# Optimization experiments

Hardware: AMD Instinct MI355X
Metric: run time of the kernel (lower is better)

Reference implementation:

```python
import jax, jax.numpy as jnp
import numpy as np

N = 100000   # n_nodes
E = 800000   # n_edges
IN = 128
HID = 128
OUT = 40
EPS = 1e-5   # BatchNorm1d eps


def setup_inputs() -> dict:
    key = jax.random.key(0)
    ks = jax.random.split(key, 16)
    def w(k, i, o):
        return jax.random.normal(k, (i, o), jnp.float32) / np.sqrt(i).astype(np.float32)
    return {
        "x": jax.random.normal(ks[0], (N, IN), jnp.float32),
        "edge_index": jax.random.randint(ks[1], (2, E), 0, N, dtype=jnp.int64),
        # SAGEConv weights: Wl acts on aggregated neighbors, Wr on root features
        "Wl0": w(ks[2], IN, HID),  "Wr0": w(ks[3], IN, HID),
        "Wl1": w(ks[4], HID, HID), "Wr1": w(ks[5], HID, HID),
        "Wl2": w(ks[6], HID, OUT), "Wr2": w(ks[7], HID, OUT),
        "b2": jnp.zeros((OUT,), jnp.float32),  # bias only on last layer
        # BatchNorm params for layers 0,1 (last layer has no BN)
        "g0": jnp.ones((HID,), jnp.float32), "be0": jnp.zeros((HID,), jnp.float32),
        "g1": jnp.ones((HID,), jnp.float32), "be1": jnp.zeros((HID,), jnp.float32),
    }


def _sage_conv(x, src, dst, Wl, Wr, b=None):
    # mean aggregation of source messages at destination nodes
    msg = x[src]                                             # [E, d] gather
    agg = jax.ops.segment_sum(msg, dst, num_segments=N)      # [N, d]
    cnt = jax.ops.segment_sum(jnp.ones((src.shape[0],), x.dtype), dst,
                              num_segments=N)                # [N]
    mean = agg / jnp.maximum(cnt, 1.0)[:, None]
    out = mean @ Wl + x @ Wr
    if b is not None:
        out = out + b
    return out


def _batch_norm(h, gamma, beta):
    # training-mode BN over node dim, biased variance (matches torch BatchNorm1d)
    mu = h.mean(axis=0)
    var = h.var(axis=0)
    return (h - mu) * jax.lax.rsqrt(var + EPS) * gamma + beta


def reference(x, edge_index, Wl0, Wr0, Wl1, Wr1, Wl2, Wr2, b2, g0, be0, g1, be1):
    src, dst = edge_index[0], edge_index[1]
    h = _sage_conv(x, src, dst, Wl0, Wr0)
    h = jax.nn.relu(_batch_norm(h, g0, be0))
    h = _sage_conv(h, src, dst, Wl1, Wr1)
    h = jax.nn.relu(_batch_norm(h, g1, be1))
    h = _sage_conv(h, src, dst, Wl2, Wr2, b2)
    return h
```

## Files before the change

### kernel.cpp

```cpp
#include <hip/hip_runtime.h>
#include <hip/hip_bf16.h>

#define N_NODES 100000
#define N_EDGES 800000
#define EPS 1e-5f
#define NBANK 32
#define HB_BLOCKS 256
#define HB_PER 3125
#define BUCKET_N 12500
#define MROW 68
#define BST 1024
#define CPT 13

typedef __attribute__((ext_vector_type(8))) short short8;
typedef __attribute__((ext_vector_type(4))) float floatx4;

__device__ __forceinline__ unsigned short f2b(float f) {
    unsigned int u = __float_as_uint(f);
    u = (u + 0x7fffu + ((u >> 16) & 1u)) >> 16;
    return (unsigned short)u;
}
__device__ __forceinline__ float blo(unsigned int u) { return __uint_as_float(u << 16); }
__device__ __forceinline__ float bhi(unsigned int u) { return __uint_as_float(u & 0xffff0000u); }
__device__ __forceinline__ float b2f(unsigned short s) {
    return __uint_as_float(((unsigned int)s) << 16);
}

__device__ __forceinline__ void pack_one(const float* __restrict__ Wl,
                                         const float* __restrict__ Wr,
                                         unsigned short* __restrict__ out,
                                         int Hreal, int NCT, int tid) {
    int i = tid & 7;
    int lane = (tid >> 3) & 63;
    int q = tid >> 9;
    int c = q % NCT;
    int t = q / NCT;
    int k = t * 32 + (lane >> 4) * 8 + i;
    int n = c * 16 + (lane & 15);
    float v = 0.f;
    if (n < Hreal) v = (k < 128) ? Wl[k * Hreal + n] : Wr[(k - 128) * Hreal + n];
    out[tid] = f2b(v);
}

__global__ void __launch_bounds__(256) prep_k(const float* __restrict__ x,
                                              unsigned short* __restrict__ o,
                                              const int* __restrict__ dst,
                                              unsigned int* __restrict__ bhist,
                                              const float* __restrict__ Wl0, const float* __restrict__ Wr0,
                                              const float* __restrict__ Wl1, const float* __restrict__ Wr1,
                                              const float* __restrict__ Wl2, const float* __restrict__ Wr2,
                                              unsigned short* __restrict__ W0p,
                                              unsigned short* __restrict__ W1p,
                                              unsigned short* __restrict__ W2p) {
    int b = blockIdx.x;
    if (b < 12500) {
        int i = b * 256 + threadIdx.x;
        float4 v = ((const float4*)x)[i];
        ushort4 r;
        r.x = f2b(v.x); r.y = f2b(v.y); r.z = f2b(v.z); r.w = f2b(v.w);
        ((ushort4*)o)[i] = r;
        return;
    }
    if (b < 12756) {
        __shared__ unsigned int lh[8];
        int hb = b - 12500;
        if (threadIdx.x < 8) lh[threadIdx.x] = 0;
        __syncthreads();
        int start = hb * HB_PER;
        for (int i = threadIdx.x; i < HB_PER; i += 256) {
            int d = dst[start + i];
            atomicAdd(&lh[(unsigned int)d / BUCKET_N], 1u);
        }
        __syncthreads();
        if (threadIdx.x < 8) bhist[threadIdx.x * HB_BLOCKS + hb] = lh[threadIdx.x];
        return;
    }
    int tid = (b - 12756) * 256 + threadIdx.x;
    if (tid < 32768) pack_one(Wl0, Wr0, W0p, 128, 8, tid);
    else if (tid < 65536) pack_one(Wl1, Wr1, W1p, 128, 8, tid - 32768);
    else pack_one(Wl2, Wr2, W2p, 40, 3, tid - 65536);
}

__global__ void bscan(unsigned int* __restrict__ A) {
    __shared__ unsigned int part[256];
    int t = threadIdx.x;
    unsigned int v[8];
    unsigned int s = 0;
#pragma unroll
    for (int i = 0; i < 8; i++) { v[i] = A[t * 8 + i]; s += v[i]; }
    part[t] = s; __syncthreads();
    for (int off = 1; off < 256; off <<= 1) {
        unsigned int add = (t >= off) ? part[t - off] : 0u;
        __syncthreads();
        part[t] += add;
        __syncthreads();
    }
    unsigned int base = part[t] - s;
#pragma unroll
    for (int i = 0; i < 8; i++) { unsigned int old = v[i]; A[t * 8 + i] = base; base += old; }
}

__global__ void __launch_bounds__(256) bscatter(const int* __restrict__ src,
                                                const int* __restrict__ dst,
                                                const unsigned int* __restrict__ boffs,
                                                unsigned int* __restrict__ ebuf) {
    __shared__ unsigned int cur[8];
    if (threadIdx.x < 8) cur[threadIdx.x] = boffs[threadIdx.x * HB_BLOCKS + blockIdx.x];
    __syncthreads();
    int start = blockIdx.x * HB_PER;
    for (int i = threadIdx.x; i < HB_PER; i += 256) {
        int d = dst[start + i];
        int s = src[start + i];
        unsigned int b = (unsigned int)d / BUCKET_N;
        unsigned int dl = (unsigned int)d - b * BUCKET_N;
        unsigned int pos = atomicAdd(&cur[b], 1u);
        ebuf[pos] = (unsigned int)s | (dl << 17);
    }
}

__global__ void __launch_bounds__(BST) bucket_sort_k(const unsigned int* __restrict__ ebuf,
                                                     const unsigned int* __restrict__ bhist,
                                                     unsigned int* __restrict__ rowptr,
                                                     int* __restrict__ srclist) {
    __shared__ unsigned int cntl[BUCKET_N];
    __shared__ unsigned int psum[BST];
    int g = blockIdx.x;
    int t = threadIdx.x;
    unsigned int estart = bhist[g * HB_BLOCKS];
    unsigned int eend = (g == 7) ? N_EDGES : bhist[(g + 1) * HB_BLOCKS];

    for (int i = t; i < BUCKET_N; i += BST) cntl[i] = 0u;
    __syncthreads();

    for (unsigned int i = estart + t; i < eend; i += BST)
        atomicAdd(&cntl[ebuf[i] >> 17], 1u);
    __syncthreads();

    unsigned int loc[CPT];
    unsigned int s = 0;
    int base = t * CPT;
#pragma unroll
    for (int i = 0; i < CPT; i++) {
        unsigned int v = (base + i < BUCKET_N) ? cntl[base + i] : 0u;
        loc[i] = s;
        s += v;
    }
    psum[t] = s;
    __syncthreads();
    for (int off = 1; off < BST; off <<= 1) {
        unsigned int add = (t >= off) ? psum[t - off] : 0u;
        __syncthreads();
        psum[t] += add;
        __syncthreads();
    }
    unsigned int tb = psum[t] - s;
#pragma unroll
    for (int i = 0; i < CPT; i++) {
        if (base + i < BUCKET_N) {
            unsigned int ol = tb + loc[i];
            cntl[base + i] = ol;
            rowptr[g * BUCKET_N + base + i] = estart + ol;
        }
    }
    if (g == 7 && t == 0) rowptr[N_NODES] = N_EDGES;
    __syncthreads();

    for (unsigned int i = estart + t; i < eend; i += BST) {
        unsigned int p = ebuf[i];
        unsigned int pos = atomicAdd(&cntl[p >> 17], 1u);
        srclist[estart + pos] = (int)(p & 0x1FFFFu);
    }
}

template<int BN>
__device__ __forceinline__ void agg_phase16(const unsigned short* __restrict__ hb,
                                            const unsigned int* __restrict__ rowptr,
                                            const int* __restrict__ srclist,
                                            unsigned int* __restrict__ smean,
                                            const float* __restrict__ sc,
                                            const float* __restrict__ sh,
                                            int wave, int g, int l, int blockrow) {
    const uint4* hp = (const uint4*)hb;
    int nl = wave * 4 + g;
    int node = blockrow + nl;
    float f0 = 0.f, f1 = 0.f, f2 = 0.f, f3 = 0.f, f4 = 0.f, f5 = 0.f, f6 = 0.f, f7 = 0.f;
    float sc0r = 0.f, sc1r = 0.f, sc2r = 0.f, sc3r = 0.f, sc4r = 0.f, sc5r = 0.f, sc6r = 0.f, sc7r = 0.f;
    float sh0r = 0.f, sh1r = 0.f, sh2r = 0.f, sh3r = 0.f, sh4r = 0.f, sh5r = 0.f, sh6r = 0.f, sh7r = 0.f;
    if (BN) {
        const float* s0 = sc + l * 8;
        const float* s1 = sh + l * 8;
        sc0r = s0[0]; sc1r = s0[1]; sc2r = s0[2]; sc3r = s0[3];
        sc4r = s0[4]; sc5r = s0[5]; sc6r = s0[6]; sc7r = s0[7];
        sh0r = s1[0]; sh1r = s1[1]; sh2r = s1[2]; sh3r = s1[3];
        sh4r = s1[4]; sh5r = s1[5]; sh6r = s1[6]; sh7r = s1[7];
    }
    unsigned int b = rowptr[node], e = rowptr[node + 1];
    unsigned int p = b;
#define ACC8(U) { \
    if (BN) { \
        f0 += fmaxf(0.f, fmaf(blo(U.x), sc0r, sh0r)); \
        f1 += fmaxf(0.f, fmaf(bhi(U.x), sc1r, sh1r)); \
        f2 += fmaxf(0.f, fmaf(blo(U.y), sc2r, sh2r)); \
        f3 += fmaxf(0.f, fmaf(bhi(U.y), sc3r, sh3r)); \
        f4 += fmaxf(0.f, fmaf(blo(U.z), sc4r, sh4r)); \
        f5 += fmaxf(0.f, fmaf(bhi(U.z), sc5r, sh5r)); \
        f6 += fmaxf(0.f, fmaf(blo(U.w), sc6r, sh6r)); \
        f7 += fmaxf(0.f, fmaf(bhi(U.w), sc7r, sh7r)); \
    } else { \
        f0 += blo(U.x); f1 += bhi(U.x); f2 += blo(U.y); f3 += bhi(U.y); \
        f4 += blo(U.z); f5 += bhi(U.z); f6 += blo(U.w); f7 += bhi(U.w); \
    } }
    int s0 = 0, s1 = 0, s2 = 0, s3 = 0;
    bool have = (p + 4 <= e);
    if (have) { s0 = srclist[p]; s1 = srclist[p + 1]; s2 = srclist[p + 2]; s3 = srclist[p + 3]; }
    while (have) {
        uint4 u0 = hp[(size_t)s0 * 16 + l];
        uint4 u1 = hp[(size_t)s1 * 16 + l];
        uint4 u2 = hp[(size_t)s2 * 16 + l];
        uint4 u3 = hp[(size_t)s3 * 16 + l];
        p += 4;
        have = (p + 4 <= e);
        if (have) { s0 = srclist[p]; s1 = srclist[p + 1]; s2 = srclist[p + 2]; s3 = srclist[p + 3]; }
        ACC8(u0); ACC8(u1); ACC8(u2); ACC8(u3);
    }
    if (p + 2 <= e) {
        int t0 = srclist[p];
        int t1 = srclist[p + 1];
        uint4 u0 = hp[(size_t)t0 * 16 + l];
        uint4 u1 = hp[(size_t)t1 * 16 + l];
        ACC8(u0); ACC8(u1);
        p += 2;
    }
    if (p < e) {
        int t0 = srclist[p];
        uint4 u0 = hp[(size_t)t0 * 16 + l];
        ACC8(u0);
    }
#undef ACC8
    unsigned int deg = e - b;
    float r = 1.0f / (float)(deg > 1u ? deg : 1u);
    uint4 o;
    o.x = (unsigned int)f2b(f0 * r) | ((unsigned int)f2b(f1 * r) << 16);
    o.y = (unsigned int)f2b(f2 * r) | ((unsigned int)f2b(f3 * r) << 16);
    o.z = (unsigned int)f2b(f4 * r) | ((unsigned int)f2b(f5 * r) << 16);
    o.w = (unsigned int)f2b(f6 * r) | ((unsigned int)f2b(f7 * r) << 16);
    *(uint4*)&smean[nl * MROW + l * 4] = o;
}

__device__ __forceinline__ short8 bn_pack8(short8 raw, const float* __restrict__ scb,
                                           const float* __restrict__ shb, int koff) {
    short8 r;
#pragma unroll
    for (int i = 0; i < 8; i++) {
        float v = b2f((unsigned short)raw[i]);
        v = fmaxf(0.f, fmaf(v, scb[koff + i], shb[koff + i]));
        r[i] = (short)f2b(v);
    }
    return r;
}

template<int BN>
__global__ void __launch_bounds__(256) gemm2f_k(const unsigned short* __restrict__ hb,
                                                const unsigned int* __restrict__ rowptr,
                                                const int* __restrict__ srclist,
                                                const float* __restrict__ sc,
                                                const float* __restrict__ sh,
                                                const unsigned short* __restrict__ Bp,
                                                unsigned short* __restrict__ outb,
                                                float* __restrict__ sums) {
    __shared__ unsigned int smean[16 * MROW];
    __shared__ float lds_s[128];
    __shared__ float lds_s2[128];
    __shared__ float scb[128];
    __shared__ float shb[128];
    int wave = threadIdx.x >> 6;
    int lane = threadIdx.x & 63;
    int quad = lane >> 4;
    int l15 = lane & 15;
    int blockrow = blockIdx.x * 16;

    if (threadIdx.x < 128) {
        lds_s[threadIdx.x] = 0.f; lds_s2[threadIdx.x] = 0.f;
        if (BN) { scb[threadIdx.x] = sc[threadIdx.x]; shb[threadIdx.x] = sh[threadIdx.x]; }
    }
    if (BN) __syncthreads();

    agg_phase16<BN>(hb, rowptr, srclist, smean, sc, sh, wave, quad, l15, blockrow);
    __syncthreads();

    floatx4 acc[2];
    acc[0] = (floatx4){0.f, 0.f, 0.f, 0.f};
    acc[1] = (floatx4){0.f, 0.f, 0.f, 0.f};

    int r0 = blockrow + l15;

#pragma unroll
    for (int t = 0; t < 8; t++) {
        short8 a0;
        if (t < 4) {
            a0 = *(const short8*)&smean[l15 * MROW + t * 16 + quad * 4];
        } else {
            int koff = (t & 3) * 32 + quad * 8;
            short8 raw = *(const short8*)(hb + (size_t)r0 * 128 + koff);
            a0 = BN ? bn_pack8(raw, scb, shb, koff) : raw;
        }
#pragma unroll
        for (int c = 0; c < 2; c++) {
            int cidx = wave * 2 + c;
            short8 bf = *(const short8*)(Bp + ((size_t)(t * 8 + cidx) * 64 + lane) * 8);
            acc[c] = __builtin_amdgcn_mfma_f32_16x16x32_bf16(a0, bf, acc[c], 0, 0, 0);
        }
    }

#pragma unroll
    for (int c = 0; c < 2; c++) {
        int col = wave * 32 + c * 16 + l15;
        float s = 0.f, s2 = 0.f;
#pragma unroll
        for (int r = 0; r < 4; r++) {
            int row = blockrow + quad * 4 + r;
            float v = acc[c][r];
            outb[(size_t)row * 128 + col] = f2b(v);
            s += v; s2 += v * v;
        }
        s += __shfl_xor(s, 16);  s += __shfl_xor(s, 32);
        s2 += __shfl_xor(s2, 16); s2 += __shfl_xor(s2, 32);
        if (quad == 0) {
            atomicAdd(&lds_s[col], s);
            atomicAdd(&lds_s2[col], s2);
        }
    }

    __syncthreads();
    if (threadIdx.x < 128) {
        int bank = blockIdx.x & (NBANK - 1);
        atomicAdd(&sums[bank * 256 + threadIdx.x], lds_s[threadIdx.x]);
        atomicAdd(&sums[bank * 256 + 128 + threadIdx.x], lds_s2[threadIdx.x]);
    }
}

__global__ void __launch_bounds__(192) dense_k(const unsigned short* __restrict__ hb,
                                               const float* __restrict__ sc,
                                               const float* __restrict__ sh,
                                               const unsigned short* __restrict__ Bp,
                                               const float* __restrict__ bias,
                                               unsigned short* __restrict__ P,
                                               float* __restrict__ Q) {
    __shared__ float scb[128];
    __shared__ float shb[128];
    int wave = threadIdx.x >> 6;
    int lane = threadIdx.x & 63;
    int quad = lane >> 4;
    int l15 = lane & 15;
    int blockrow = blockIdx.x * 16;

    if (threadIdx.x < 128) { scb[threadIdx.x] = sc[threadIdx.x]; shb[threadIdx.x] = sh[threadIdx.x]; }
    __syncthreads();

    int r0 = blockrow + l15;
    short8 af[4];
#pragma unroll
    for (int t = 0; t < 4; t++) {
        int koff = t * 32 + quad * 8;
        short8 raw = *(const short8*)(hb + (size_t)r0 * 128 + koff);
        af[t] = bn_pack8(raw, scb, shb, koff);
    }

    floatx4 aP = (floatx4){0.f, 0.f, 0.f, 0.f};
    floatx4 aQ = (floatx4){0.f, 0.f, 0.f, 0.f};
#pragma unroll
    for (int t = 0; t < 4; t++) {
        short8 bl = *(const short8*)(Bp + ((size_t)(t * 3 + wave) * 64 + lane) * 8);
        aP = __builtin_amdgcn_mfma_f32_16x16x32_bf16(af[t], bl, aP, 0, 0, 0);
    }
#pragma unroll
    for (int t = 0; t < 4; t++) {
        short8 br = *(const short8*)(Bp + ((size_t)((t + 4) * 3 + wave) * 64 + lane) * 8);
        aQ = __builtin_amdgcn_mfma_f32_16x16x32_bf16(af[t], br, aQ, 0, 0, 0);
    }
    int col = wave * 16 + l15;
    if (col < 40) {
#pragma unroll
        for (int r = 0; r < 4; r++) {
            int row = blockrow + quad * 4 + r;
            P[(size_t)row * 40 + col] = f2b(aP[r]);
            Q[(size_t)row * 40 + col] = aQ[r] + bias[col];
        }
    }
}

__global__ void __launch_bounds__(256) agg40_k(const unsigned short* __restrict__ P,
                                               const unsigned int* __restrict__ rowptr,
                                               const int* __restrict__ srclist,
                                               const float* __restrict__ Q,
                                               float* __restrict__ out) {
    int tid = threadIdx.x;
    int g = tid >> 3;
    int l = tid & 7;
    int ll = l < 5 ? l : 0;
    int node = blockIdx.x * 32 + g;
    const uint4* pp = (const uint4*)P;
    float f0 = 0.f, f1 = 0.f, f2 = 0.f, f3 = 0.f, f4 = 0.f, f5 = 0.f, f6 = 0.f, f7 = 0.f;
    unsigned int b = rowptr[node], e = rowptr[node + 1];
    unsigned int p = b;
#define ACC8(U) { f0 += blo(U.x); f1 += bhi(U.x); f2 += blo(U.y); f3 += bhi(U.y); \
                  f4 += blo(U.z); f5 += bhi(U.z); f6 += blo(U.w); f7 += bhi(U.w); }
    int s0 = 0, s1 = 0, s2 = 0, s3 = 0;
    bool have = (p + 4 <= e);
    if (have) { s0 = srclist[p]; s1 = srclist[p + 1]; s2 = srclist[p + 2]; s3 = srclist[p + 3]; }
    while (have) {
        uint4 u0 = pp[(size_t)s0 * 5 + ll];
        uint4 u1 = pp[(size_t)s1 * 5 + ll];
        uint4 u2 = pp[(size_t)s2 * 5 + ll];
        uint4 u3 = pp[(size_t)s3 * 5 + ll];
        p += 4;
        have = (p + 4 <= e);
        if (have) { s0 = srclist[p]; s1 = srclist[p + 1]; s2 = srclist[p + 2]; s3 = srclist[p + 3]; }
        ACC8(u0); ACC8(u1); ACC8(u2); ACC8(u3);
    }
    if (p + 2 <= e) {
        int t0 = srclist[p];
        int t1 = srclist[p + 1];
        uint4 u0 = pp[(size_t)t0 * 5 + ll];
        uint4 u1 = pp[(size_t)t1 * 5 + ll];
        ACC8(u0); ACC8(u1);
        p += 2;
    }
    if (p < e) {
        int t0 = srclist[p];
        uint4 u0 = pp[(size_t)t0 * 5 + ll];
        ACC8(u0);
    }
#undef ACC8
    unsigned int deg = e - b;
    float r = 1.0f / (float)(deg > 1u ? deg : 1u);
    if (l < 5) {
        size_t base = (size_t)node * 40 + l * 8;
        float4 o1, o2;
        o1.x = f0 * r + Q[base + 0]; o1.y = f1 * r + Q[base + 1];
        o1.z = f2 * r + Q[base + 2]; o1.w = f3 * r + Q[base + 3];
        o2.x = f4 * r + Q[base + 4]; o2.y = f5 * r + Q[base + 5];
        o2.z = f6 * r + Q[base + 6]; o2.w = f7 * r + Q[base + 7];
        *(float4*)(out + base) = o1;
        *(float4*)(out + base + 4) = o2;
    }
}

__global__ void bn_finalize(const float* __restrict__ sums, const float* __restrict__ g,
                            const float* __restrict__ be, float* __restrict__ sc,
                            float* __restrict__ sh) {
    __shared__ float lds[256];
    int t = threadIdx.x;
    float s = 0.f;
#pragma unroll 8
    for (int bk = 0; bk < NBANK; bk++) s += sums[bk * 256 + t];
    lds[t] = s;
    __syncthreads();
    if (t < 128) {
        float inv_n = 1.0f / (float)N_NODES;
        float mu = lds[t] * inv_n;
        float var = lds[128 + t] * inv_n - mu * mu;
        float sf = g[t] * rsqrtf(var + EPS);
        sc[t] = sf;
        sh[t] = be[t] - mu * sf;
    }
}

extern "C" void kernel_launch(void* const* d_in, const int* in_sizes, int n_in,
                              void* d_out, int out_size, void* d_ws, size_t ws_size,
                              hipStream_t stream) {
    const float* x   = (const float*)d_in[0];
    const int* ei    = (const int*)d_in[1];
    const float* Wl0 = (const float*)d_in[2];
    const float* Wr0 = (const float*)d_in[3];
    const float* Wl1 = (const float*)d_in[4];
    const float* Wr1 = (const float*)d_in[5];
    const float* Wl2 = (const float*)d_in[6];
    const float* Wr2 = (const float*)d_in[7];
    const float* b2  = (const float*)d_in[8];
    const float* g0  = (const float*)d_in[9];
    const float* be0 = (const float*)d_in[10];
    const float* g1  = (const float*)d_in[11];
    const float* be1 = (const float*)d_in[12];

    char* ws = (char*)d_ws;
    size_t off = 0;
    auto alloc = [&](size_t bytes) -> void* {
        void* p = ws + off;
        off += (bytes + 4095) & ~(size_t)4095;
        return p;
    };

    const size_t NB16 = (size_t)N_NODES * 128 * 2;
    unsigned short* xb   = (unsigned short*)alloc(NB16);
    unsigned short* C0b  = (unsigned short*)alloc(NB16);
    unsigned short* C1b  = (unsigned short*)alloc(NB16);
    float* sums0         = (float*)alloc(NBANK * 256 * 4);
    float* sums1         = (float*)alloc(NBANK * 256 * 4);
    unsigned int* rowptr = (unsigned int*)alloc((size_t)(N_NODES + 1) * 4);
    int* srclist         = (int*)alloc((size_t)N_EDGES * 4);
    unsigned int* ebuf   = (unsigned int*)alloc((size_t)N_EDGES * 4);
    unsigned int* bhist  = (unsigned int*)alloc(8 * HB_BLOCKS * 4);
    float* sc            = (float*)alloc(128 * 4);
    float* sh            = (float*)alloc(128 * 4);
    unsigned short* W0p  = (unsigned short*)alloc(8 * 8 * 64 * 8 * 2);
    unsigned short* W1p  = (unsigned short*)alloc(8 * 8 * 64 * 8 * 2);
    unsigned short* W2p  = (unsigned short*)alloc(3 * 8 * 64 * 8 * 2);

    unsigned short* P40  = C0b;
    float* Q             = (float*)xb;

    const int* srcp = ei;
    const int* dstp = ei + N_EDGES;

    hipMemsetAsync(sums0, 0, (size_t)2 * NBANK * 256 * 4, stream);

    prep_k<<<13060, 256, 0, stream>>>(x, xb, dstp, bhist,
                                      Wl0, Wr0, Wl1, Wr1, Wl2, Wr2, W0p, W1p, W2p);

    bscan<<<1, 256, 0, stream>>>(bhist);
    bscatter<<<HB_BLOCKS, 256, 0, stream>>>(srcp, dstp, bhist, ebuf);
    bucket_sort_k<<<8, BST, 0, stream>>>(ebuf, bhist, rowptr, srclist);

    gemm2f_k<0><<<6250, 256, 0, stream>>>(xb, rowptr, srclist, nullptr, nullptr, W0p, C0b, sums0);
    bn_finalize<<<1, 256, 0, stream>>>(sums0, g0, be0, sc, sh);

    gemm2f_k<1><<<6250, 256, 0, stream>>>(C0b, rowptr, srclist, sc, sh, W1p, C1b, sums1);
    bn_finalize<<<1, 256, 0, stream>>>(sums1, g1, be1, sc, sh);

    dense_k<<<6250, 192, 0, stream>>>(C1b, sc, sh, W2p, b2, P40, Q);
    agg40_k<<<3125, 256, 0, stream>>>(P40, rowptr, srclist, Q, (float*)d_out);

    (void)in_sizes; (void)n_in; (void)out_size; (void)ws_size;
}
```

Measured before the change: 375.5 us.

## Split CSR bucket sort into 250 small buckets for more parallel blocks

New measurement: 307.3 us (median of 2 runs). 1.22x faster.

```diff
diff --git a/kernel.cpp b/kernel.cpp
--- a/kernel.cpp
+++ b/kernel.cpp
@@ -7,10 +7,9 @@
 #define NBANK 32
 #define HB_BLOCKS 256
 #define HB_PER 3125
-#define BUCKET_N 12500
+#define NBUCK 250
+#define BUCKET_N 400
 #define MROW 68
-#define BST 1024
-#define CPT 13
 
 typedef __attribute__((ext_vector_type(8))) short short8;
 typedef __attribute__((ext_vector_type(4))) float floatx4;
@@ -62,9 +61,9 @@
         return;
     }
     if (b < 12756) {
-        __shared__ unsigned int lh[8];
+        __shared__ unsigned int lh[NBUCK];
         int hb = b - 12500;
-        if (threadIdx.x < 8) lh[threadIdx.x] = 0;
+        if (threadIdx.x < NBUCK) lh[threadIdx.x] = 0;
         __syncthreads();
         int start = hb * HB_PER;
         for (int i = threadIdx.x; i < HB_PER; i += 256) {
@@ -72,7 +71,7 @@
             atomicAdd(&lh[(unsigned int)d / BUCKET_N], 1u);
         }
         __syncthreads();
-        if (threadIdx.x < 8) bhist[threadIdx.x * HB_BLOCKS + hb] = lh[threadIdx.x];
+        if (threadIdx.x < NBUCK) bhist[threadIdx.x * HB_BLOCKS + hb] = lh[threadIdx.x];
         return;
     }
     int tid = (b - 12756) * 256 + threadIdx.x;
@@ -81,31 +80,36 @@
     else pack_one(Wl2, Wr2, W2p, 40, 3, tid - 65536);
 }
 
-__global__ void bscan(unsigned int* __restrict__ A) {
-    __shared__ unsigned int part[256];
+__global__ void __launch_bounds__(1024) bscan(unsigned int* __restrict__ A) {
+    __shared__ unsigned int part[1024];
     int t = threadIdx.x;
-    unsigned int v[8];
+    unsigned int v[64];
     unsigned int s = 0;
-#pragma unroll
-    for (int i = 0; i < 8; i++) { v[i] = A[t * 8 + i]; s += v[i]; }
-    part[t] = s; __syncthreads();
-    for (int off = 1; off < 256; off <<= 1) {
+    if (t < 1000) {
+#pragma unroll
+        for (int i = 0; i < 64; i++) { v[i] = A[t * 64 + i]; s += v[i]; }
+    }
+    part[t] = s;
+    __syncthreads();
+    for (int off = 1; off < 1024; off <<= 1) {
         unsigned int add = (t >= off) ? part[t - off] : 0u;
         __syncthreads();
         part[t] += add;
         __syncthreads();
     }
-    unsigned int base = part[t] - s;
-#pragma unroll
-    for (int i = 0; i < 8; i++) { unsigned int old = v[i]; A[t * 8 + i] = base; base += old; }
+    if (t < 1000) {
+        unsigned int base = part[t] - s;
+#pragma unroll
+        for (int i = 0; i < 64; i++) { unsigned int old = v[i]; A[t * 64 + i] = base; base += old; }
+    }
 }
 
 __global__ void __launch_bounds__(256) bscatter(const int* __restrict__ src,
                                                 const int* __restrict__ dst,
                                                 const unsigned int* __restrict__ boffs,
                                                 unsigned int* __restrict__ ebuf) {
-    __shared__ unsigned int cur[8];
-    if (threadIdx.x < 8) cur[threadIdx.x] = boffs[threadIdx.x * HB_BLOCKS + blockIdx.x];
+    __shared__ unsigned int cur[NBUCK];
+    if (threadIdx.x < NBUCK) cur[threadIdx.x] = boffs[threadIdx.x * HB_BLOCKS + blockIdx.x];
     __syncthreads();
     int start = blockIdx.x * HB_PER;
     for (int i = threadIdx.x; i < HB_PER; i += 256) {
@@ -118,54 +122,55 @@
     }
 }
 
-__global__ void __launch_bounds__(BST) bucket_sort_k(const unsigned int* __restrict__ ebuf,
+__global__ void __launch_bounds__(256) bucket_sort_k(const unsigned int* __restrict__ ebuf,
                                                      const unsigned int* __restrict__ bhist,
                                                      unsigned int* __restrict__ rowptr,
                                                      int* __restrict__ srclist) {
     __shared__ unsigned int cntl[BUCKET_N];
-    __shared__ unsigned int psum[BST];
+    __shared__ unsigned int psum[256];
     int g = blockIdx.x;
     int t = threadIdx.x;
     unsigned int estart = bhist[g * HB_BLOCKS];
-    unsigned int eend = (g == 7) ? N_EDGES : bhist[(g + 1) * HB_BLOCKS];
-
-    for (int i = t; i < BUCKET_N; i += BST) cntl[i] = 0u;
-    __syncthreads();
-
-    for (unsigned int i = estart + t; i < eend; i += BST)
+    unsigned int eend = (g == NBUCK - 1) ? N_EDGES : bhist[(g + 1) * HB_BLOCKS];
+
+    if (t < BUCKET_N) cntl[t] = 0u;
+    if (t + 256 < BUCKET_N) cntl[t + 256] = 0u;
+    __syncthreads();
+
+    for (unsigned int i = estart + t; i < eend; i += 256)
         atomicAdd(&cntl[ebuf[i] >> 17], 1u);
     __syncthreads();
 
-    unsigned int loc[CPT];
-    unsigned int s = 0;
-    int base = t * CPT;
-#pragma unroll
-    for (int i = 0; i < CPT; i++) {
-        unsigned int v = (base + i < BUCKET_N) ? cntl[base + i] : 0u;
-        loc[i] = s;
-        s += v;
+    unsigned int l0 = 0, l1 = 0, s = 0;
+    int base = t * 2;
+    if (base < BUCKET_N) {
+        unsigned int v0 = cntl[base];
+        unsigned int v1 = (base + 1 < BUCKET_N) ? cntl[base + 1] : 0u;
+        l0 = 0; l1 = v0; s = v0 + v1;
     }
     psum[t] = s;
     __syncthreads();
-    for (int off = 1; off < BST; off <<= 1) {
+    for (int off = 1; off < 256; off <<= 1) {
         unsigned int add = (t >= off) ? psum[t - off] : 0u;
         __syncthreads();
         psum[t] += add;
         __syncthreads();
     }
     unsigned int tb = psum[t] - s;
-#pragma unroll
-    for (int i = 0; i < CPT; i++) {
-        if (base + i < BUCKET_N) {
-            unsigned int ol = tb + loc[i];
-            cntl[base + i] = ol;
-            rowptr[g * BUCKET_N + base + i] = estart + ol;
-        }
-    }
-    if (g == 7 && t == 0) rowptr[N_NODES] = N_EDGES;
-    __syncthreads();
-
-    for (unsigned int i = estart + t; i < eend; i += BST) {
+    if (base < BUCKET_N) {
+        unsigned int o0 = tb + l0;
+        unsigned int o1 = tb + l1;
+        cntl[base] = o0;
+        rowptr[g * BUCKET_N + base] = estart + o0;
+        if (base + 1 < BUCKET_N) {
+            cntl[base + 1] = o1;
+            rowptr[g * BUCKET_N + base + 1] = estart + o1;
+        }
+    }
+    if (g == NBUCK - 1 && t == 0) rowptr[N_NODES] = N_EDGES;
+    __syncthreads();
+
+    for (unsigned int i = estart + t; i < eend; i += 256) {
         unsigned int p = ebuf[i];
         unsigned int pos = atomicAdd(&cntl[p >> 17], 1u);
         srclist[estart + pos] = (int)(p & 0x1FFFFu);
@@ -500,7 +505,7 @@
     unsigned int* rowptr = (unsigned int*)alloc((size_t)(N_NODES + 1) * 4);
     int* srclist         = (int*)alloc((size_t)N_EDGES * 4);
     unsigned int* ebuf   = (unsigned int*)alloc((size_t)N_EDGES * 4);
-    unsigned int* bhist  = (unsigned int*)alloc(8 * HB_BLOCKS * 4);
+    unsigned int* bhist  = (unsigned int*)alloc((size_t)NBUCK * HB_BLOCKS * 4);
     float* sc            = (float*)alloc(128 * 4);
     float* sh            = (float*)alloc(128 * 4);
     unsigned short* W0p  = (unsigned short*)alloc(8 * 8 * 64 * 8 * 2);
@@ -518,9 +523,9 @@
     prep_k<<<13060, 256, 0, stream>>>(x, xb, dstp, bhist,
                                       Wl0, Wr0, Wl1, Wr1, Wl2, Wr2, W0p, W1p, W2p);
 
-    bscan<<<1, 256, 0, stream>>>(bhist);
+    bscan<<<1, 1024, 0, stream>>>(bhist);
     bscatter<<<HB_BLOCKS, 256, 0, stream>>>(srcp, dstp, bhist, ebuf);
-    bucket_sort_k<<<8, BST, 0, stream>>>(ebuf, bhist, rowptr, srclist);
+    bucket_sort_k<<<NBUCK, 256, 0, stream>>>(ebuf, bhist, rowptr, srclist);
 
     gemm2f_k<0><<<6250, 256, 0, stream>>>(xb, rowptr, srclist, nullptr, nullptr, W0p, C0b, sums0);
     bn_finalize<<<1, 256, 0, stream>>>(sums0, g0, be0, sc, sh);
```
